# Kernel tuning notes

Hardware: AMD Instinct MI355X
Metric: run time of the kernel (lower is better)

Reference implementation:

```python
import math
import jax, jax.numpy as jnp
import numpy as np

D = 1024
H = 16
DK = D // H
B = 4
L = 2048


def setup_inputs() -> dict:
    key = jax.random.key(0)
    ks = jax.random.split(key, 11)
    s = 1.0 / math.sqrt(D)
    return {
        "q": jax.random.normal(ks[0], (B, L, D), jnp.float32),
        "k": jax.random.normal(ks[1], (B, L, D), jnp.float32),
        "v": jax.random.normal(ks[2], (B, L, D), jnp.float32),
        "wq_w": jax.random.normal(ks[3], (D, D), jnp.float32) * s,
        "wq_b": jnp.zeros((D,), jnp.float32),
        "wk_w": jax.random.normal(ks[4], (D, D), jnp.float32) * s,
        "wk_b": jnp.zeros((D,), jnp.float32),
        "wv_w": jax.random.normal(ks[5], (D, D), jnp.float32) * s,
        "wv_b": jnp.zeros((D,), jnp.float32),
        "wo_w": jax.random.normal(ks[6], (D, D), jnp.float32) * s,
        "wo_b": jnp.zeros((D,), jnp.float32),
    }


def reference(q, k, v, wq_w, wq_b, wk_w, wk_b, wv_w, wv_b, wo_w, wo_b):
    # torch Linear: x @ W.T + b
    Q = (q @ wq_w.T + wq_b).reshape(B, L, H, DK).transpose(0, 2, 1, 3)  # [B,H,L,DK]
    K = (k @ wk_w.T + wk_b).reshape(B, -1, H, DK).transpose(0, 2, 1, 3)
    V = (v @ wv_w.T + wv_b).reshape(B, -1, H, DK).transpose(0, 2, 1, 3)
    sc = jnp.einsum("bhqd,bhkd->bhqk", Q, K) / math.sqrt(DK)  # [B,H,L,L]
    # causal mask: strictly upper triangular filled with -1e9
    cm = jnp.triu(jnp.ones((L, L), dtype=bool), 1)
    sc = jnp.where(cm, jnp.float32(-1e9), sc)
    at = jax.nn.softmax(sc, axis=-1)  # dropout p=0 (eval)
    out = jnp.einsum("bhqk,bhkd->bhqd", at, V)  # [B,H,L,DK]
    out = out.transpose(0, 2, 1, 3).reshape(B, L, D)
    return out @ wo_w.T + wo_b
```

## Files before the change

kernel.cpp:

```cpp
#include <hip/hip_runtime.h>
#include <stdint.h>

#define DD 1024
#define NH 16
#define DHEAD 64
#define NB 4
#define SEQ 2048
#define MR (NB*SEQ)
#define NT (SEQ/128)

typedef __attribute__((ext_vector_type(8))) short s8v;
typedef __attribute__((ext_vector_type(4))) float f4v;

__device__ __forceinline__ unsigned short f2bf(float f) {
  union { float f; uint32_t u; } c; c.f = f;
  uint32_t u = c.u;
  u += 0x7fffu + ((u >> 16) & 1u);
  return (unsigned short)(u >> 16);
}
__device__ __forceinline__ unsigned short f2bf_trunc(float f) {
  union { float f; uint32_t u; } c; c.f = f;
  return (unsigned short)(c.u >> 16);
}

__device__ __forceinline__ void load_lds16(const void* g, void* lds) {
  __builtin_amdgcn_global_load_lds(
      (__attribute__((address_space(1))) void*)(uintptr_t)g,
      (__attribute__((address_space(3))) void*)(uint32_t)(uintptr_t)lds,
      16, 0, 0);
}

__global__ void cvt_w(
    const float* __restrict__ w0, const float* __restrict__ w1,
    const float* __restrict__ w2, const float* __restrict__ w3,
    unsigned short* __restrict__ d0, unsigned short* __restrict__ d1,
    unsigned short* __restrict__ d2, unsigned short* __restrict__ d3)
{
  int blk = blockIdx.x;
  int a = blk >> 9;
  const float* src = a == 0 ? w0 : (a == 1 ? w1 : (a == 2 ? w2 : w3));
  unsigned short* dst = a == 0 ? d0 : (a == 1 ? d1 : (a == 2 ? d2 : d3));
  size_t i = (size_t)(blk & 511) * 2048 + (size_t)threadIdx.x * 8;
  float4 a4 = *(const float4*)(src + i);
  float4 b4 = *(const float4*)(src + i + 4);
  union { unsigned short us[8]; uint4 u; } t;
  t.us[0] = f2bf(a4.x); t.us[1] = f2bf(a4.y); t.us[2] = f2bf(a4.z); t.us[3] = f2bf(a4.w);
  t.us[4] = f2bf(b4.x); t.us[5] = f2bf(b4.y); t.us[6] = f2bf(b4.z); t.us[7] = f2bf(b4.w);
  *(uint4*)(dst + i) = t.u;
}

__global__ void cvt_a(
    const float* __restrict__ s0, const float* __restrict__ s1,
    const float* __restrict__ s2,
    unsigned short* __restrict__ d0, unsigned short* __restrict__ d1,
    unsigned short* __restrict__ d2)
{
  int blk = blockIdx.x;
  int a = blk >> 12;
  const float* src = a == 0 ? s0 : (a == 1 ? s1 : s2);
  unsigned short* dst = a == 0 ? d0 : (a == 1 ? d1 : d2);
  size_t i = (size_t)(blk & 4095) * 2048 + (size_t)threadIdx.x * 8;
  float4 a4 = *(const float4*)(src + i);
  float4 b4 = *(const float4*)(src + i + 4);
  union { unsigned short us[8]; uint4 u; } t;
  t.us[0] = f2bf(a4.x); t.us[1] = f2bf(a4.y); t.us[2] = f2bf(a4.z); t.us[3] = f2bf(a4.w);
  t.us[4] = f2bf(b4.x); t.us[5] = f2bf(b4.y); t.us[6] = f2bf(b4.z); t.us[7] = f2bf(b4.w);
  *(uint4*)(dst + i) = t.u;
}

__global__ __launch_bounds__(256, 2) void gemm_bt(
    const unsigned short* __restrict__ A,
    const unsigned short* __restrict__ Bw,
    const float* __restrict__ bias,
    float* __restrict__ Cout)
{
  __shared__ __align__(16) short As[128 * 64];
  __shared__ __align__(16) short Bs[128 * 64];
  const int linear = blockIdx.y * 8 + blockIdx.x;
  const int nx = linear >> 6;
  const int my = linear & 63;
  const int tid = threadIdx.x;
  const int wave = tid >> 6, lane = tid & 63;
  const int wm = (wave >> 1) * 64, wn = (wave & 1) * 64;
  const int lr = lane & 15, lg = lane >> 4;
  const int sw = lr & 7;
  const unsigned short* Ab = A + (size_t)my * 128 * DD;
  const unsigned short* Bb = Bw + (size_t)nx * 128 * DD;

  f4v z = {0.f, 0.f, 0.f, 0.f};
  f4v acc[4][4];
  for (int mi = 0; mi < 4; mi++) for (int ni = 0; ni < 4; ni++) acc[mi][ni] = z;

  for (int k0 = 0; k0 < DD; k0 += 64) {
    __syncthreads();
    for (int i = 0; i < 4; i++) {
      int c = tid + i * 256;
      int row = c >> 3, pg = c & 7;
      load_lds16(Ab + (size_t)row * DD + k0 + ((pg ^ (row & 7)) << 3), As + c * 8);
    }
    for (int i = 0; i < 4; i++) {
      int c = tid + i * 256;
      int row = c >> 3, pg = c & 7;
      load_lds16(Bb + (size_t)row * DD + k0 + ((pg ^ (row & 7)) << 3), Bs + c * 8);
    }
    __syncthreads();
    for (int kk = 0; kk < 64; kk += 32) {
      int gb = kk >> 3;
      s8v af[4], bf[4];
      for (int i = 0; i < 4; i++)
        af[i] = *(const s8v*)(As + (wm + i * 16 + lr) * 64 + (((gb + lg) ^ sw) << 3));
      for (int i = 0; i < 4; i++)
        bf[i] = *(const s8v*)(Bs + (wn + i * 16 + lr) * 64 + (((gb + lg) ^ sw) << 3));
      for (int mi = 0; mi < 4; mi++)
        for (int ni = 0; ni < 4; ni++)
          acc[mi][ni] = __builtin_amdgcn_mfma_f32_16x16x32_bf16(af[mi], bf[ni], acc[mi][ni], 0, 0, 0);
    }
  }
  for (int ni = 0; ni < 4; ni++) {
    int col = nx * 128 + wn + ni * 16 + lr;
    float bv = bias[col];
    for (int mi = 0; mi < 4; mi++) {
      int row0 = my * 128 + wm + mi * 16 + lg * 4;
      for (int r = 0; r < 4; r++)
        Cout[(size_t)(row0 + r) * DD + col] = acc[mi][ni][r] + bv;
    }
  }
}

__global__ __launch_bounds__(256, 2) void gemm_qkv(
    const unsigned short* __restrict__ qA, const unsigned short* __restrict__ kA,
    const unsigned short* __restrict__ vA,
    const unsigned short* __restrict__ wq, const unsigned short* __restrict__ wk,
    const unsigned short* __restrict__ wv,
    const float* __restrict__ bq, const float* __restrict__ bk, const float* __restrict__ bv,
    unsigned short* __restrict__ Qp, unsigned short* __restrict__ Kp,
    unsigned short* __restrict__ VpT)
{
  __shared__ __align__(16) short As[128 * 64];
  __shared__ __align__(16) short Bs[128 * 64];
  const int linear = blockIdx.y * 24 + blockIdx.x;
  const int nx  = linear / 192;
  const int rem = linear % 192;
  const int seg = rem >> 6;
  const int my  = rem & 63;
  const unsigned short* A  = seg == 0 ? qA : (seg == 1 ? kA : vA);
  const unsigned short* Bw = seg == 0 ? wq : (seg == 1 ? wk : wv);
  const float* bias        = seg == 0 ? bq : (seg == 1 ? bk : bv);

  const int tid = threadIdx.x;
  const int wave = tid >> 6, lane = tid & 63;
  const int wm = (wave >> 1) * 64, wn = (wave & 1) * 64;
  const int lr = lane & 15, lg = lane >> 4;
  const int sw = lr & 7;
  const unsigned short* Ab = A + (size_t)my * 128 * DD;
  const unsigned short* Bb = Bw + (size_t)nx * 128 * DD;

  f4v z = {0.f, 0.f, 0.f, 0.f};
  f4v acc[4][4];
  for (int mi = 0; mi < 4; mi++) for (int ni = 0; ni < 4; ni++) acc[mi][ni] = z;

  for (int k0 = 0; k0 < DD; k0 += 64) {
    __syncthreads();
    for (int i = 0; i < 4; i++) {
      int c = tid + i * 256;
      int row = c >> 3, pg = c & 7;
      load_lds16(Ab + (size_t)row * DD + k0 + ((pg ^ (row & 7)) << 3), As + c * 8);
    }
    for (int i = 0; i < 4; i++) {
      int c = tid + i * 256;
      int row = c >> 3, pg = c & 7;
      load_lds16(Bb + (size_t)row * DD + k0 + ((pg ^ (row & 7)) << 3), Bs + c * 8);
    }
    __syncthreads();
    for (int kk = 0; kk < 64; kk += 32) {
      int gb = kk >> 3;
      s8v af[4], bf[4];
      for (int i = 0; i < 4; i++)
        af[i] = *(const s8v*)(As + (wm + i * 16 + lr) * 64 + (((gb + lg) ^ sw) << 3));
      for (int i = 0; i < 4; i++)
        bf[i] = *(const s8v*)(Bs + (wn + i * 16 + lr) * 64 + (((gb + lg) ^ sw) << 3));
      for (int mi = 0; mi < 4; mi++)
        for (int ni = 0; ni < 4; ni++)
          acc[mi][ni] = __builtin_amdgcn_mfma_f32_16x16x32_bf16(af[mi], bf[ni], acc[mi][ni], 0, 0, 0);
    }
  }
  if (seg < 2) {
    unsigned short* Cout = seg == 0 ? Qp : Kp;
    for (int ni = 0; ni < 4; ni++) {
      int col = nx * 128 + wn + ni * 16 + lr;
      float bv = bias[col];
      for (int mi = 0; mi < 4; mi++) {
        int row0 = my * 128 + wm + mi * 16 + lg * 4;
        for (int r = 0; r < 4; r++)
          Cout[(size_t)(row0 + r) * DD + col] = f2bf(acc[mi][ni][r] + bv);
      }
    }
  } else {
    for (int ni = 0; ni < 4; ni++) {
      int col = nx * 128 + wn + ni * 16 + lr;
      float bv = bias[col];
      int hh = col >> 6, dd = col & 63;
      for (int mi = 0; mi < 4; mi++) {
        int row0 = my * 128 + wm + mi * 16 + lg * 4;
        int bb = row0 >> 11, ll = row0 & 2047;
        uint64_t w = 0;
        for (int r = 0; r < 4; r++)
          w |= (uint64_t)f2bf(acc[mi][ni][r] + bv) << (16 * r);
        *(uint64_t*)(VpT + ((size_t)(bb * NH + hh) * 64 + dd) * SEQ + ll) = w;
      }
    }
  }
}

#define KS_STRIDE 72
#define VT_STRIDE 136
#define PS_STRIDE 72

__device__ __forceinline__ void attn_step(
    const s8v (&qf)[2][2], const s8v (&kf)[2][4],
    f4v (&o)[2][4], float (&ls)[2][4],
    int qbase, int colbase,
    const short* __restrict__ Vt, int vsub, short* __restrict__ Pw,
    int lr, int lg)
{
  const float csc = 0.125f * 1.44269504089f;
  const float FM = 14.0f;
  f4v zv = {0.f, 0.f, 0.f, 0.f};
  f4v s[2][4];
  for (int mi = 0; mi < 2; mi++) for (int ni = 0; ni < 4; ni++) s[mi][ni] = zv;
  for (int ks = 0; ks < 2; ks++)
    for (int mi = 0; mi < 2; mi++)
      for (int ni = 0; ni < 4; ni++)
        s[mi][ni] = __builtin_amdgcn_mfma_f32_16x16x32_bf16(qf[mi][ks], kf[ks][ni], s[mi][ni], 0, 0, 0);
  const bool diag = (colbase + 63 > qbase);
  for (int mi = 0; mi < 2; mi++)
    for (int ni = 0; ni < 4; ni++)
      for (int r = 0; r < 4; r++) {
        float e = __builtin_amdgcn_exp2f(fmaf(s[mi][ni][r], csc, -FM));
        if (diag) {
          int row = qbase + mi * 16 + lg * 4 + r;
          int col = colbase + ni * 16 + lr;
          e = (col > row) ? 0.f : e;
        }
        ls[mi][r] += e;
        Pw[(mi * 16 + lg * 4 + r) * PS_STRIDE + ni * 16 + lr] = (short)f2bf_trunc(e);
      }
  for (int kc2 = 0; kc2 < 2; kc2++) {
    s8v pf[2], vf[4];
    for (int mi = 0; mi < 2; mi++)
      pf[mi] = *(const s8v*)(Pw + (mi * 16 + lr) * PS_STRIDE + kc2 * 32 + lg * 8);
    for (int ni = 0; ni < 4; ni++)
      vf[ni] = *(const s8v*)(Vt + (ni * 16 + lr) * VT_STRIDE + vsub + kc2 * 32 + lg * 8);
    for (int mi = 0; mi < 2; mi++)
      for (int ni = 0; ni < 4; ni++)
        o[mi][ni] = __builtin_amdgcn_mfma_f32_16x16x32_bf16(pf[mi], vf[ni], o[mi][ni], 0, 0, 0);
  }
}

__global__ __launch_bounds__(256, 2) void fattn(
    const unsigned short* __restrict__ Qp,
    const unsigned short* __restrict__ Kp,
    const unsigned short* __restrict__ VpT,
    unsigned short* __restrict__ Op)
{
  __shared__ __align__(16) short Ks[128 * KS_STRIDE];
  __shared__ __align__(16) short Vt[64 * VT_STRIDE];
  __shared__ __align__(16) short Ps[4 * 32 * PS_STRIDE];
  const int tid = threadIdx.x;
  const int wave = tid >> 6, lane = tid & 63;
  const int lr = lane & 15, lg = lane >> 4;
  const int linear = blockIdx.y * 8 + blockIdx.x;
  const int xA = linear >> 6;
  const int bh = linear & 63;
  const int b = bh >> 4, h = bh & 15;
  const int xB = NT - 1 - xA;
  const int qbA = xA * 128 + wave * 32;
  const int qbB = xB * 128 + wave * 32;
  const unsigned short* Qrow = Qp + ((size_t)b * SEQ) * DD + h * DHEAD;
  const unsigned short* Krow = Kp + ((size_t)b * SEQ) * DD + h * DHEAD;
  const unsigned short* VT   = VpT + (size_t)bh * 64 * SEQ;
  short* Pw = Ps + wave * (32 * PS_STRIDE);

  s8v qfA[2][2], qfB[2][2];
  for (int mi = 0; mi < 2; mi++)
    for (int ks = 0; ks < 2; ks++) {
      qfA[mi][ks] = *(const s8v*)(Qrow + (size_t)(qbA + mi * 16 + lr) * DD + ks * 32 + lg * 8);
      qfB[mi][ks] = *(const s8v*)(Qrow + (size_t)(qbB + mi * 16 + lr) * DD + ks * 32 + lg * 8);
    }

  f4v zv = {0.f, 0.f, 0.f, 0.f};
  f4v oA[2][4], oB[2][4];
  float lA[2][4], lB[2][4];
  for (int mi = 0; mi < 2; mi++)
    for (int r = 0; r < 4; r++) { lA[mi][r] = 0.f; lB[mi][r] = 0.f; }
  for (int mi = 0; mi < 2; mi++)
    for (int ni = 0; ni < 4; ni++) { oA[mi][ni] = zv; oB[mi][ni] = zv; }

  const int npair = xB + 1;

  for (int p = 0; p < npair; p++) {
    s8v kreg[4], vreg[4];
    int krow[4], kkc[4], vd[4], vkc[4];
    for (int i = 0; i < 4; i++) {
      int c = tid + i * 256;
      krow[i] = c >> 3; kkc[i] = (c & 7) << 3;
      kreg[i] = *(const s8v*)(Krow + (size_t)(p * 128 + krow[i]) * DD + kkc[i]);
      vd[i] = c >> 4; vkc[i] = (c & 15) << 3;
      vreg[i] = *(const s8v*)(VT + (size_t)vd[i] * SEQ + p * 128 + vkc[i]);
    }
    __syncthreads();
    for (int i = 0; i < 4; i++) {
      *(s8v*)(Ks + krow[i] * KS_STRIDE + kkc[i]) = kreg[i];
      *(s8v*)(Vt + vd[i] * VT_STRIDE + vkc[i]) = vreg[i];
    }
    __syncthreads();
    for (int sub = 0; sub < 2; sub++) {
      int colbase = (2 * p + sub) * 64;
      bool actB = colbase <= qbB + 31;
      bool actA = colbase <= qbA + 31;
      if (actB || actA) {
        const short* KsSub = Ks + sub * 64 * KS_STRIDE;
        s8v kf[2][4];
        for (int ks = 0; ks < 2; ks++)
          for (int ni = 0; ni < 4; ni++)
            kf[ks][ni] = *(const s8v*)(KsSub + (ni * 16 + lr) * KS_STRIDE + ks * 32 + lg * 8);
        int vsub = sub * 64;
        if (actB) attn_step(qfB, kf, oB, lB, qbB, colbase, Vt, vsub, Pw, lr, lg);
        if (actA) attn_step(qfA, kf, oA, lA, qbA, colbase, Vt, vsub, Pw, lr, lg);
      }
    }
  }

  unsigned short* Orow = Op + ((size_t)b * SEQ) * DD + h * DHEAD;
  for (int mi = 0; mi < 2; mi++)
    for (int r = 0; r < 4; r++) {
      float sA = lA[mi][r], sB = lB[mi][r];
      for (int d2 = 1; d2 < 16; d2 <<= 1) {
        sA += __shfl_xor(sA, d2);
        sB += __shfl_xor(sB, d2);
      }
      float invA = 1.f / sA, invB = 1.f / sB;
      size_t rowA = (size_t)qbA + mi * 16 + lg * 4 + r;
      size_t rowB = (size_t)qbB + mi * 16 + lg * 4 + r;
      for (int ni = 0; ni < 4; ni++) {
        Orow[rowA * DD + ni * 16 + lr] = f2bf(oA[mi][ni][r] * invA);
        Orow[rowB * DD + ni * 16 + lr] = f2bf(oB[mi][ni][r] * invB);
      }
    }
}

extern "C" void kernel_launch(void* const* d_in, const int* in_sizes, int n_in,
                              void* d_out, int out_size, void* d_ws, size_t ws_size,
                              hipStream_t stream) {
  const float* q    = (const float*)d_in[0];
  const float* k    = (const float*)d_in[1];
  const float* v    = (const float*)d_in[2];
  const float* wq_w = (const float*)d_in[3];
  const float* wq_b = (const float*)d_in[4];
  const float* wk_w = (const float*)d_in[5];
  const float* wk_b = (const float*)d_in[6];
  const float* wv_w = (const float*)d_in[7];
  const float* wv_b = (const float*)d_in[8];
  const float* wo_w = (const float*)d_in[9];
  const float* wo_b = (const float*)d_in[10];

  const size_t BIG = (size_t)MR * DD;
  const size_t WSZ = (size_t)DD * DD;
  unsigned short* p = (unsigned short*)d_ws;
  unsigned short* wqb = p; p += WSZ;
  unsigned short* wkb = p; p += WSZ;
  unsigned short* wvb = p; p += WSZ;
  unsigned short* wob = p; p += WSZ;
  unsigned short* Qp  = p; p += BIG;
  unsigned short* Kp  = p; p += BIG;
  unsigned short* VpT = p; p += BIG;
  unsigned short* AO  = p; p += BIG;

  unsigned short* qb = AO;
  unsigned short* kb = (unsigned short*)d_out;
  unsigned short* vb = kb + BIG;

  cvt_w<<<dim3(2048), dim3(256), 0, stream>>>(
      wq_w, wk_w, wv_w, wo_w, wqb, wkb, wvb, wob);

  cvt_a<<<dim3(12288), dim3(256), 0, stream>>>(q, k, v, qb, kb, vb);

  gemm_qkv<<<dim3(24, MR / 128), dim3(256), 0, stream>>>(
      qb, kb, vb, wqb, wkb, wvb, wq_b, wk_b, wv_b, Qp, Kp, VpT);

  fattn<<<dim3(NT / 2, NB * NH), dim3(256), 0, stream>>>(Qp, Kp, VpT, AO);

  gemm_bt<<<dim3(8, MR / 128), dim3(256), 0, stream>>>(AO, wob, wo_b, (float*)d_out);

  (void)in_sizes; (void)n_in; (void)out_size; (void)ws_size;
}
```

Measured before the change: 314.0 us.

## Prefetch next K/V tile in attention, split P buffers, add MFMA priority, merge convert kernels

```diff
diff --git a/kernel.cpp b/kernel.cpp
--- a/kernel.cpp
+++ b/kernel.cpp
@@ -30,36 +30,32 @@
       16, 0, 0);
 }
 
-__global__ void cvt_w(
+__global__ void cvt_all(
     const float* __restrict__ w0, const float* __restrict__ w1,
     const float* __restrict__ w2, const float* __restrict__ w3,
-    unsigned short* __restrict__ d0, unsigned short* __restrict__ d1,
-    unsigned short* __restrict__ d2, unsigned short* __restrict__ d3)
+    const float* __restrict__ a0, const float* __restrict__ a1,
+    const float* __restrict__ a2,
+    unsigned short* __restrict__ dw0, unsigned short* __restrict__ dw1,
+    unsigned short* __restrict__ dw2, unsigned short* __restrict__ dw3,
+    unsigned short* __restrict__ da0, unsigned short* __restrict__ da1,
+    unsigned short* __restrict__ da2)
 {
   int blk = blockIdx.x;
-  int a = blk >> 9;
-  const float* src = a == 0 ? w0 : (a == 1 ? w1 : (a == 2 ? w2 : w3));
-  unsigned short* dst = a == 0 ? d0 : (a == 1 ? d1 : (a == 2 ? d2 : d3));
-  size_t i = (size_t)(blk & 511) * 2048 + (size_t)threadIdx.x * 8;
-  float4 a4 = *(const float4*)(src + i);
-  float4 b4 = *(const float4*)(src + i + 4);
-  union { unsigned short us[8]; uint4 u; } t;
-  t.us[0] = f2bf(a4.x); t.us[1] = f2bf(a4.y); t.us[2] = f2bf(a4.z); t.us[3] = f2bf(a4.w);
-  t.us[4] = f2bf(b4.x); t.us[5] = f2bf(b4.y); t.us[6] = f2bf(b4.z); t.us[7] = f2bf(b4.w);
-  *(uint4*)(dst + i) = t.u;
-}
-
-__global__ void cvt_a(
-    const float* __restrict__ s0, const float* __restrict__ s1,
-    const float* __restrict__ s2,
-    unsigned short* __restrict__ d0, unsigned short* __restrict__ d1,
-    unsigned short* __restrict__ d2)
-{
-  int blk = blockIdx.x;
-  int a = blk >> 12;
-  const float* src = a == 0 ? s0 : (a == 1 ? s1 : s2);
-  unsigned short* dst = a == 0 ? d0 : (a == 1 ? d1 : d2);
-  size_t i = (size_t)(blk & 4095) * 2048 + (size_t)threadIdx.x * 8;
+  const float* src;
+  unsigned short* dst;
+  size_t i;
+  if (blk < 2048) {
+    int a = blk >> 9;
+    src = a == 0 ? w0 : (a == 1 ? w1 : (a == 2 ? w2 : w3));
+    dst = a == 0 ? dw0 : (a == 1 ? dw1 : (a == 2 ? dw2 : dw3));
+    i = (size_t)(blk & 511) * 2048 + (size_t)threadIdx.x * 8;
+  } else {
+    int blk2 = blk - 2048;
+    int a = blk2 >> 12;
+    src = a == 0 ? a0 : (a == 1 ? a1 : a2);
+    dst = a == 0 ? da0 : (a == 1 ? da1 : da2);
+    i = (size_t)(blk2 & 4095) * 2048 + (size_t)threadIdx.x * 8;
+  }
   float4 a4 = *(const float4*)(src + i);
   float4 b4 = *(const float4*)(src + i + 4);
   union { unsigned short us[8]; uint4 u; } t;
@@ -228,10 +224,12 @@
   f4v zv = {0.f, 0.f, 0.f, 0.f};
   f4v s[2][4];
   for (int mi = 0; mi < 2; mi++) for (int ni = 0; ni < 4; ni++) s[mi][ni] = zv;
+  __builtin_amdgcn_s_setprio(1);
   for (int ks = 0; ks < 2; ks++)
     for (int mi = 0; mi < 2; mi++)
       for (int ni = 0; ni < 4; ni++)
         s[mi][ni] = __builtin_amdgcn_mfma_f32_16x16x32_bf16(qf[mi][ks], kf[ks][ni], s[mi][ni], 0, 0, 0);
+  __builtin_amdgcn_s_setprio(0);
   const bool diag = (colbase + 63 > qbase);
   for (int mi = 0; mi < 2; mi++)
     for (int ni = 0; ni < 4; ni++)
@@ -251,9 +249,11 @@
       pf[mi] = *(const s8v*)(Pw + (mi * 16 + lr) * PS_STRIDE + kc2 * 32 + lg * 8);
     for (int ni = 0; ni < 4; ni++)
       vf[ni] = *(const s8v*)(Vt + (ni * 16 + lr) * VT_STRIDE + vsub + kc2 * 32 + lg * 8);
+    __builtin_amdgcn_s_setprio(1);
     for (int mi = 0; mi < 2; mi++)
       for (int ni = 0; ni < 4; ni++)
         o[mi][ni] = __builtin_amdgcn_mfma_f32_16x16x32_bf16(pf[mi], vf[ni], o[mi][ni], 0, 0, 0);
+    __builtin_amdgcn_s_setprio(0);
   }
 }
 
@@ -265,7 +265,7 @@
 {
   __shared__ __align__(16) short Ks[128 * KS_STRIDE];
   __shared__ __align__(16) short Vt[64 * VT_STRIDE];
-  __shared__ __align__(16) short Ps[4 * 32 * PS_STRIDE];
+  __shared__ __align__(16) short Ps[8 * 32 * PS_STRIDE];
   const int tid = threadIdx.x;
   const int wave = tid >> 6, lane = tid & 63;
   const int lr = lane & 15, lg = lane >> 4;
@@ -279,7 +279,8 @@
   const unsigned short* Qrow = Qp + ((size_t)b * SEQ) * DD + h * DHEAD;
   const unsigned short* Krow = Kp + ((size_t)b * SEQ) * DD + h * DHEAD;
   const unsigned short* VT   = VpT + (size_t)bh * 64 * SEQ;
-  short* Pw = Ps + wave * (32 * PS_STRIDE);
+  short* PwB = Ps + wave * (64 * PS_STRIDE);
+  short* PwA = PwB + 32 * PS_STRIDE;
 
   s8v qfA[2][2], qfB[2][2];
   for (int mi = 0; mi < 2; mi++)
@@ -298,22 +299,31 @@
 
   const int npair = xB + 1;
 
+  int krow[4], kkc[4], vd[4], vkc[4];
+  for (int i = 0; i < 4; i++) {
+    int c = tid + i * 256;
+    krow[i] = c >> 3; kkc[i] = (c & 7) << 3;
+    vd[i] = c >> 4; vkc[i] = (c & 15) << 3;
+  }
+  s8v kreg[4], vreg[4];
+  for (int i = 0; i < 4; i++) {
+    kreg[i] = *(const s8v*)(Krow + (size_t)krow[i] * DD + kkc[i]);
+    vreg[i] = *(const s8v*)(VT + (size_t)vd[i] * SEQ + vkc[i]);
+  }
+
   for (int p = 0; p < npair; p++) {
-    s8v kreg[4], vreg[4];
-    int krow[4], kkc[4], vd[4], vkc[4];
-    for (int i = 0; i < 4; i++) {
-      int c = tid + i * 256;
-      krow[i] = c >> 3; kkc[i] = (c & 7) << 3;
-      kreg[i] = *(const s8v*)(Krow + (size_t)(p * 128 + krow[i]) * DD + kkc[i]);
-      vd[i] = c >> 4; vkc[i] = (c & 15) << 3;
-      vreg[i] = *(const s8v*)(VT + (size_t)vd[i] * SEQ + p * 128 + vkc[i]);
-    }
     __syncthreads();
     for (int i = 0; i < 4; i++) {
       *(s8v*)(Ks + krow[i] * KS_STRIDE + kkc[i]) = kreg[i];
       *(s8v*)(Vt + vd[i] * VT_STRIDE + vkc[i]) = vreg[i];
     }
     __syncthreads();
+    if (p + 1 < npair) {
+      for (int i = 0; i < 4; i++) {
+        kreg[i] = *(const s8v*)(Krow + (size_t)((p + 1) * 128 + krow[i]) * DD + kkc[i]);
+        vreg[i] = *(const s8v*)(VT + (size_t)vd[i] * SEQ + (p + 1) * 128 + vkc[i]);
+      }
+    }
     for (int sub = 0; sub < 2; sub++) {
       int colbase = (2 * p + sub) * 64;
       bool actB = colbase <= qbB + 31;
@@ -325,8 +335,8 @@
           for (int ni = 0; ni < 4; ni++)
             kf[ks][ni] = *(const s8v*)(KsSub + (ni * 16 + lr) * KS_STRIDE + ks * 32 + lg * 8);
         int vsub = sub * 64;
-        if (actB) attn_step(qfB, kf, oB, lB, qbB, colbase, Vt, vsub, Pw, lr, lg);
-        if (actA) attn_step(qfA, kf, oA, lA, qbA, colbase, Vt, vsub, Pw, lr, lg);
+        if (actB) attn_step(qfB, kf, oB, lB, qbB, colbase, Vt, vsub, PwB, lr, lg);
+        if (actA) attn_step(qfA, kf, oA, lA, qbA, colbase, Vt, vsub, PwA, lr, lg);
       }
     }
   }
@@ -380,10 +390,9 @@
   unsigned short* kb = (unsigned short*)d_out;
   unsigned short* vb = kb + BIG;
 
-  cvt_w<<<dim3(2048), dim3(256), 0, stream>>>(
-      wq_w, wk_w, wv_w, wo_w, wqb, wkb, wvb, wob);
-
-  cvt_a<<<dim3(12288), dim3(256), 0, stream>>>(q, k, v, qb, kb, vb);
+  cvt_all<<<dim3(14336), dim3(256), 0, stream>>>(
+      wq_w, wk_w, wv_w, wo_w, q, k, v,
+      wqb, wkb, wvb, wob, qb, kb, vb);
 
   gemm_qkv<<<dim3(24, MR / 128), dim3(256), 0, stream>>>(
       qb, kb, vb, wqb, wkb, wvb, wq_b, wk_b, wv_b, Qp, Kp, VpT);
```

After: 321.6 us. 1.02x slower.
